# Optimization experiments

Measured on AMD Instinct MI355X. Metric: run time of the kernel, lower is better.

The kernel has to match this reference:

```python
import jax, jax.numpy as jnp
import numpy as np

N, E = 50000, 800000
IN_FEATS, EDGE_FEATS = 256, 64
H, F = 8, 32  # num_heads, out_feats
LRELU_SLOPE = 0.01  # nn.LeakyReLU() default (module ignores alpha arg)


def setup_inputs() -> dict:
    key = jax.random.key(0)
    ks = jax.random.split(key, 9)
    return {
        "h": jax.random.normal(ks[0], (N, IN_FEATS), jnp.float32),
        "edge_features": jax.random.normal(ks[1], (E, EDGE_FEATS), jnp.float32),
        "src": jax.random.randint(ks[2], (E,), 0, N, jnp.int32),
        "dst": jax.random.randint(ks[3], (E,), 0, N, jnp.int32),
        "W_w": jax.random.normal(ks[4], (IN_FEATS, H * F), jnp.float32) * 0.05,
        "We_w": jax.random.normal(ks[5], (EDGE_FEATS, H * F), jnp.float32) * 0.05,
        "a_src": jax.random.normal(ks[6], (H, F), jnp.float32) * 0.1,
        "a_dst": jax.random.normal(ks[7], (H, F), jnp.float32) * 0.1,
        "a_edge": jax.random.normal(ks[8], (H, F), jnp.float32) * 0.1,
    }


def reference(h, edge_features, src, dst, W_w, We_w, a_src, a_dst, a_edge):
    # Node / edge linear projections -> [N,H,F], [E,H,F]
    Wh = (h @ W_w).reshape(-1, H, F)
    We = (edge_features @ We_w).reshape(-1, H, F)

    # Per-edge attention logits [E,H]: score = src.a_src + dst.a_dst + e.a_edge
    s = (jnp.einsum('ehf,hf->eh', Wh[src], a_src)
         + jnp.einsum('ehf,hf->eh', Wh[dst], a_dst)
         + jnp.einsum('ehf,hf->eh', We, a_edge))
    s = jnp.where(s > 0, s, LRELU_SLOPE * s)

    # Segment softmax over incoming edges of each dst node
    m = jax.ops.segment_max(s, dst, num_segments=N)          # [N,H]
    ex = jnp.exp(s - m[dst])                                 # [E,H]
    den = jax.ops.segment_sum(ex, dst, num_segments=N)       # [N,H]
    a = ex / den[dst]                                        # [E,H]

    # Weighted scatter-sum aggregation (dropout is identity at p=0 / eval)
    msg = Wh[src] * a[:, :, None]                            # [E,H,F]
    h_new = jax.ops.segment_sum(msg, dst, num_segments=N)    # [N,H,F]

    # concat=True path: reshape + ELU
    h_new = h_new.reshape(-1, H * F)
    return jax.nn.elu(h_new)
```

## Files before the change

### kernel.cpp

```cpp
#include <hip/hip_runtime.h>
#include <hip/hip_fp16.h>

#define N_NODES 50000
#define N_EDGES 800000
#define HEADS 8
#define FOUT 32
#define HF 256
#define IN_F 256
#define EDGE_F 64
#define SCAN_BLOCKS 196
#define HIST_BLOCKS 3125
#define CVTW_BLOCKS 256

typedef __attribute__((ext_vector_type(8))) short bf16x8;
typedef __attribute__((ext_vector_type(4))) float f32x4;

__device__ inline ushort f2bf(float f) {
  unsigned u = __float_as_uint(f);
  unsigned r = 0x7FFFu + ((u >> 16) & 1u);
  return (ushort)((u + r) >> 16);
}

__global__ __launch_bounds__(256) void k_misc(
    const int* __restrict__ dst, int* __restrict__ deg,
    const float* __restrict__ W, ushort* __restrict__ Wt,
    const float* __restrict__ We_w, const float* __restrict__ a_edge,
    float* __restrict__ Bmat)
{
  int b = blockIdx.x;
  if (b < HIST_BLOCKS) {
    int e = b * 256 + threadIdx.x;
    atomicAdd(&deg[dst[e]], 1);
  } else if (b < HIST_BLOCKS + CVTW_BLOCKS) {
    int i = (b - HIST_BLOCKS) * 256 + threadIdx.x;
    int n = i >> 8, k = i & 255;
    Wt[i] = f2bf(W[k * HF + n]);
  } else {
    int i = (b - HIST_BLOCKS - CVTW_BLOCKS) * 256 + threadIdx.x;
    if (i < EDGE_F * HEADS) {
      int k = i >> 3, h = i & 7;
      float s = 0.f;
#pragma unroll
      for (int f = 0; f < FOUT; ++f)
        s += We_w[k * HF + h * FOUT + f] * a_edge[h * FOUT + f];
      Bmat[i] = s;
    }
  }
}

__global__ __launch_bounds__(256) void k_gemm_fused(
    const float* __restrict__ A,
    const ushort* __restrict__ Wt,
    const float* __restrict__ a_src, const float* __restrict__ a_dst,
    ushort* __restrict__ Whb,
    float* __restrict__ alpha_s, float* __restrict__ alpha_d, int M)
{
  __shared__ ushort As[64 * 40];
  __shared__ ushort Bs[256 * 40];
  const int tid = threadIdx.x;
  const int wave = tid >> 6, lane = tid & 63;
  const int m0 = blockIdx.x * 64;
  const int row16 = lane & 15;
  const int kg = lane >> 4;
  f32x4 acc[4][4] = {};

  const int a_r = tid >> 2;
  const int a_c = (tid & 3) * 8;
  const int a_row = m0 + a_r;

  for (int k0 = 0; k0 < IN_F; k0 += 32) {
    uint4 av = make_uint4(0, 0, 0, 0);
    if (a_row < M) {
      float4 f0 = *(const float4*)&A[(size_t)a_row * IN_F + k0 + a_c];
      float4 f1 = *(const float4*)&A[(size_t)a_row * IN_F + k0 + a_c + 4];
      av.x = (unsigned)f2bf(f0.x) | ((unsigned)f2bf(f0.y) << 16);
      av.y = (unsigned)f2bf(f0.z) | ((unsigned)f2bf(f0.w) << 16);
      av.z = (unsigned)f2bf(f1.x) | ((unsigned)f2bf(f1.y) << 16);
      av.w = (unsigned)f2bf(f1.z) | ((unsigned)f2bf(f1.w) << 16);
    }
    *(uint4*)&As[a_r * 40 + a_c] = av;
    const uint4* bp = (const uint4*)&Wt[(size_t)tid * IN_F + k0];
    uint4 b0 = bp[0], b1 = bp[1];
    *(uint4*)&Bs[tid * 40 + 0] = b0;
    *(uint4*)&Bs[tid * 40 + 8] = b1;
    uint4 b2 = bp[2], b3 = bp[3];
    *(uint4*)&Bs[tid * 40 + 16] = b2;
    *(uint4*)&Bs[tid * 40 + 24] = b3;
    __syncthreads();
    bf16x8 af[4], bfr[4];
#pragma unroll
    for (int mi = 0; mi < 4; ++mi)
      af[mi] = *(const bf16x8*)&As[(mi * 16 + row16) * 40 + kg * 8];
#pragma unroll
    for (int ni = 0; ni < 4; ++ni)
      bfr[ni] = *(const bf16x8*)&Bs[(wave * 64 + ni * 16 + row16) * 40 + kg * 8];
#pragma unroll
    for (int mi = 0; mi < 4; ++mi)
#pragma unroll
      for (int ni = 0; ni < 4; ++ni)
        acc[mi][ni] = __builtin_amdgcn_mfma_f32_16x16x32_bf16(af[mi], bfr[ni], acc[mi][ni], 0, 0, 0);
    __syncthreads();
  }

  float cs[4], cd[4];
#pragma unroll
  for (int ni = 0; ni < 4; ++ni) {
    int hh = 2 * wave + (ni >> 1);
    int ff = (ni & 1) * 16 + row16;
    cs[ni] = a_src[hh * FOUT + ff];
    cd[ni] = a_dst[hh * FOUT + ff];
  }
#pragma unroll
  for (int mi = 0; mi < 4; ++mi) {
#pragma unroll
    for (int r = 0; r < 4; ++r) {
      int row = m0 + mi * 16 + kg * 4 + r;
      float ps0 = acc[mi][0][r] * cs[0] + acc[mi][1][r] * cs[1];
      float ps1 = acc[mi][2][r] * cs[2] + acc[mi][3][r] * cs[3];
      float pd0 = acc[mi][0][r] * cd[0] + acc[mi][1][r] * cd[1];
      float pd1 = acc[mi][2][r] * cd[2] + acc[mi][3][r] * cd[3];
#pragma unroll
      for (int msk = 1; msk <= 8; msk <<= 1) {
        ps0 += __shfl_xor(ps0, msk, 64);
        ps1 += __shfl_xor(ps1, msk, 64);
        pd0 += __shfl_xor(pd0, msk, 64);
        pd1 += __shfl_xor(pd1, msk, 64);
      }
      if (row16 == 0 && row < M) {
        *(float2*)&alpha_s[row * 8 + 2 * wave] = make_float2(ps0, ps1);
        *(float2*)&alpha_d[row * 8 + 2 * wave] = make_float2(pd0, pd1);
      }
      if (row < M) {
#pragma unroll
        for (int ni = 0; ni < 4; ++ni)
          Whb[(size_t)row * HF + wave * 64 + ni * 16 + row16] = f2bf(acc[mi][ni][r]);
      }
    }
  }
}

__global__ __launch_bounds__(256) void k_scanA(const int* __restrict__ deg,
                                               int* __restrict__ blockSums)
{
  __shared__ int ws[4];
  int idx = blockIdx.x * 256 + threadIdx.x;
  int v = (idx < N_NODES) ? deg[idx] : 0;
  int s = v;
#pragma unroll
  for (int off = 32; off > 0; off >>= 1)
    s += __shfl_xor(s, off, 64);
  if ((threadIdx.x & 63) == 0) ws[threadIdx.x >> 6] = s;
  __syncthreads();
  if (threadIdx.x == 0)
    blockSums[blockIdx.x] = ws[0] + ws[1] + ws[2] + ws[3];
}

__global__ __launch_bounds__(256) void k_scanC(const int* __restrict__ deg,
                                               const int* __restrict__ blockSums,
                                               int* __restrict__ offsets,
                                               int* __restrict__ cursor)
{
  __shared__ int tmp[256];
  __shared__ int s_base;
  int t = threadIdx.x;
  int v = (t < SCAN_BLOCKS) ? blockSums[t] : 0;
  tmp[t] = v;
  __syncthreads();
  int x = v;
  for (int off = 1; off < 256; off <<= 1) {
    int y = (t >= off) ? tmp[t - off] : 0;
    __syncthreads();
    x += y;
    tmp[t] = x;
    __syncthreads();
  }
  if (t == (int)blockIdx.x) s_base = x - v;
  if (blockIdx.x == 0 && t == 255) offsets[N_NODES] = x;
  __syncthreads();
  int base = s_base;
  int idx = blockIdx.x * 256 + t;
  int d = (idx < N_NODES) ? deg[idx] : 0;
  tmp[t] = d;
  __syncthreads();
  int x2 = d;
  for (int off = 1; off < 256; off <<= 1) {
    int y = (t >= off) ? tmp[t - off] : 0;
    __syncthreads();
    x2 += y;
    tmp[t] = x2;
    __syncthreads();
  }
  if (idx < N_NODES) {
    int pre = base + x2 - d;
    offsets[idx] = pre;
    cursor[idx] = pre;
  }
}

__global__ __launch_bounds__(256) void k_sedge(
    const float* __restrict__ ef, const int* __restrict__ src,
    const int* __restrict__ dst, const float* __restrict__ alpha_s,
    const float* __restrict__ alpha_d, const float* __restrict__ Bmat,
    int* __restrict__ cursor, uint* __restrict__ s16u,
    int* __restrict__ srcN)
{
  __shared__ float Bs[EDGE_F * HEADS];
  for (int i = threadIdx.x; i < EDGE_F * HEADS; i += 256) Bs[i] = Bmat[i];
  __syncthreads();
  const int t = threadIdx.x;
  const int q = t & 3;
  const int e = blockIdx.x * 64 + (t >> 2);
  const int sn = src[e], dn = dst[e];

  float sc[8] = {};
  const float4* efr = (const float4*)&ef[(size_t)e * EDGE_F + q * 16];
#pragma unroll
  for (int g = 0; g < 4; ++g) {
    float4 v = efr[g];
    const float* b0 = &Bs[(q * 16 + g * 4) * 8];
#pragma unroll
    for (int hh = 0; hh < 8; ++hh)
      sc[hh] += v.x * b0[hh] + v.y * b0[8 + hh] + v.z * b0[16 + hh] + v.w * b0[24 + hh];
  }
#pragma unroll
  for (int hh = 0; hh < 8; ++hh) {
    sc[hh] += __shfl_xor(sc[hh], 1, 64);
    sc[hh] += __shfl_xor(sc[hh], 2, 64);
  }
  float2 as = *(const float2*)&alpha_s[sn * 8 + 2 * q];
  float2 ad = *(const float2*)&alpha_d[dn * 8 + 2 * q];
  float a0 = sc[2 * q] + as.x + ad.x;
  float a1 = sc[2 * q + 1] + as.y + ad.y;
  a0 = a0 > 0.f ? a0 : 0.01f * a0;
  a1 = a1 > 0.f ? a1 : 0.01f * a1;
  uint hv = (uint)__half_as_ushort(__float2half_rn(a0)) |
            ((uint)__half_as_ushort(__float2half_rn(a1)) << 16);
  int p = 0;
  if (q == 0) p = atomicAdd(&cursor[dn], 1);
  p = __shfl(p, t & 60, 64);
  s16u[(size_t)p * 4 + q] = hv;
  if (q == 0) srcN[p] = sn;
}

__global__ __launch_bounds__(256) void k_agg(
    const ushort* __restrict__ s16, const int* __restrict__ srcN,
    const int* __restrict__ offsets, const uint* __restrict__ Whb_u,
    float* __restrict__ out)
{
  const int n = blockIdx.x * 4 + (threadIdx.x >> 6);
  const int l = threadIdx.x & 63;
  const int beg = offsets[n], end = offsets[n + 1];
  const int es = l >> 3;
  const int h0 = l >> 4;
  const int h1 = 4 + h0;

  float m_run = -3.0e38f, l_run = 0.f;
  float acc00 = 0.f, acc01 = 0.f, acc10 = 0.f, acc11 = 0.f;

  int rx = 0;
  float s_cur = -3.0e38f;
  if (beg + es < end) {
    rx = srcN[beg + es];
    s_cur = __half2float(((const __half*)s16)[(size_t)beg * 8 + l]);
  }

  for (int c0 = beg; c0 < end; c0 += 8) {
    const int cnt = min(8, end - c0);
    int rx_n = 0;
    float s_n = -3.0e38f;
    if (c0 + 8 + es < end) {
      rx_n = srcN[c0 + 8 + es];
      s_n = __half2float(((const __half*)s16)[(size_t)(c0 + 8) * 8 + l]);
    }
    float s = s_cur;
    float mc = s;
    mc = fmaxf(mc, __shfl_xor(mc, 8, 64));
    mc = fmaxf(mc, __shfl_xor(mc, 16, 64));
    mc = fmaxf(mc, __shfl_xor(mc, 32, 64));
    float m_new = fmaxf(m_run, mc);
    float f = __expf(m_run - m_new);
    float w = __expf(s - m_new);
    float ws = w;
    ws += __shfl_xor(ws, 8, 64);
    ws += __shfl_xor(ws, 16, 64);
    ws += __shfl_xor(ws, 32, 64);
    l_run = l_run * f + ws;
    m_run = m_new;
    float f0 = __shfl(f, h0, 64);
    float f1 = __shfl(f, h1, 64);
    acc00 *= f0; acc01 *= f0; acc10 *= f1; acc11 *= f1;
    if (cnt == 8) {
#pragma unroll
      for (int k = 0; k < 8; ++k) {
        int idx = __shfl(rx, k << 3, 64);
        float w0 = __shfl(w, (k << 3) | h0, 64);
        float w1 = __shfl(w, (k << 3) | h1, 64);
        const uint* rowp = Whb_u + ((size_t)idx << 7);
        uint v0 = rowp[l];
        uint v1 = rowp[l + 64];
        acc00 = fmaf(w0, __uint_as_float(v0 << 16), acc00);
        acc01 = fmaf(w0, __uint_as_float(v0 & 0xFFFF0000u), acc01);
        acc10 = fmaf(w1, __uint_as_float(v1 << 16), acc10);
        acc11 = fmaf(w1, __uint_as_float(v1 & 0xFFFF0000u), acc11);
      }
    } else {
      for (int k = 0; k < cnt; ++k) {
        int idx = __shfl(rx, k << 3, 64);
        float w0 = __shfl(w, (k << 3) | h0, 64);
        float w1 = __shfl(w, (k << 3) | h1, 64);
        const uint* rowp = Whb_u + ((size_t)idx << 7);
        uint v0 = rowp[l];
        uint v1 = rowp[l + 64];
        acc00 = fmaf(w0, __uint_as_float(v0 << 16), acc00);
        acc01 = fmaf(w0, __uint_as_float(v0 & 0xFFFF0000u), acc01);
        acc10 = fmaf(w1, __uint_as_float(v1 << 16), acc10);
        acc11 = fmaf(w1, __uint_as_float(v1 & 0xFFFF0000u), acc11);
      }
    }
    rx = rx_n;
    s_cur = s_n;
  }

  float l0 = __shfl(l_run, h0, 64);
  float l1 = __shfl(l_run, h1, 64);
  float inv0 = (l0 > 0.f) ? 1.f / l0 : 0.f;
  float inv1 = (l1 > 0.f) ? 1.f / l1 : 0.f;
  acc00 *= inv0; acc01 *= inv0; acc10 *= inv1; acc11 *= inv1;

  float2 oA, oB;
  oA.x = acc00 > 0.f ? acc00 : expm1f(acc00);
  oA.y = acc01 > 0.f ? acc01 : expm1f(acc01);
  oB.x = acc10 > 0.f ? acc10 : expm1f(acc10);
  oB.y = acc11 > 0.f ? acc11 : expm1f(acc11);
  *(float2*)&out[(size_t)n * HF + 2 * l] = oA;
  *(float2*)&out[(size_t)n * HF + 128 + 2 * l] = oB;
}

extern "C" void kernel_launch(void* const* d_in, const int* in_sizes, int n_in,
                              void* d_out, int out_size, void* d_ws, size_t ws_size,
                              hipStream_t stream)
{
  const float* h    = (const float*)d_in[0];
  const float* ef   = (const float*)d_in[1];
  const int*   src  = (const int*)d_in[2];
  const int*   dst  = (const int*)d_in[3];
  const float* W_w  = (const float*)d_in[4];
  const float* We_w = (const float*)d_in[5];
  const float* a_s  = (const float*)d_in[6];
  const float* a_d  = (const float*)d_in[7];
  const float* a_e  = (const float*)d_in[8];
  float* out = (float*)d_out;

  char* ws = (char*)d_ws;
  size_t off = 0;
  auto take = [&](size_t bytes) {
    char* p = ws + off;
    off += (bytes + 255) & ~(size_t)255;
    return p;
  };
  ushort* Whb     = (ushort*)take((size_t)N_NODES * HF * 2);
  uint*   s16u    = (uint*)take((size_t)N_EDGES * 8 * 2);
  float* alpha_s  = (float*)take((size_t)N_NODES * HEADS * 4);
  float* alpha_d  = (float*)take((size_t)N_NODES * HEADS * 4);
  int*   srcN     = (int*)take((size_t)N_EDGES * 4);
  int*   deg      = (int*)take((size_t)N_NODES * 4);
  int*   offs     = (int*)take((size_t)(N_NODES + 1) * 4);
  int*   cursor   = (int*)take((size_t)N_NODES * 4);
  float* Bmat     = (float*)take((size_t)EDGE_F * HEADS * 4);
  ushort* Wt      = (ushort*)take((size_t)HF * IN_F * 2);
  int*   blockSums= (int*)take((size_t)SCAN_BLOCKS * 4);

  (void)hipMemsetAsync(deg, 0, N_NODES * sizeof(int), stream);
  k_misc<<<HIST_BLOCKS + CVTW_BLOCKS + 2, 256, 0, stream>>>(dst, deg, W_w, Wt,
                                                            We_w, a_e, Bmat);
  k_scanA<<<SCAN_BLOCKS, 256, 0, stream>>>(deg, blockSums);
  k_scanC<<<SCAN_BLOCKS, 256, 0, stream>>>(deg, blockSums, offs, cursor);
  k_gemm_fused<<<(N_NODES + 63) / 64, 256, 0, stream>>>(h, Wt, a_s, a_d, Whb,
                                                        alpha_s, alpha_d, N_NODES);
  k_sedge<<<N_EDGES / 64, 256, 0, stream>>>(ef, src, dst, alpha_s, alpha_d,
                                            Bmat, cursor, s16u, srcN);
  k_agg<<<N_NODES / 4, 256, 0, stream>>>((const ushort*)s16u, srcN, offs,
                                         (const uint*)Whb, out);
}
```

Measured before the change: 242.8 us.

## Fuse scan-A into GEMM launch, process two edges per thread, widen agg loads

The block-sum scan kernel is folded into the GEMM launch as extra blocks, which removes one kernel launch and lets the scan overlap with GEMM work. The edge-score kernel now handles two edges per thread group, halving its grid and adding memory-level parallelism at the cost of more registers. The aggregation kernel maps each lane to four contiguous features of one head and uses 8-byte loads with one float4 store, replacing two strided 4-byte loads and two float2 stores. This cuts shuffle and instruction count per edge.

```diff
diff --git a/kernel.cpp b/kernel.cpp
--- a/kernel.cpp
+++ b/kernel.cpp
@@ -11,6 +11,7 @@
 #define SCAN_BLOCKS 196
 #define HIST_BLOCKS 3125
 #define CVTW_BLOCKS 256
+#define GEMM_BLOCKS 782
 
 typedef __attribute__((ext_vector_type(8))) short bf16x8;
 typedef __attribute__((ext_vector_type(4))) float f32x4;
@@ -53,8 +54,25 @@
     const ushort* __restrict__ Wt,
     const float* __restrict__ a_src, const float* __restrict__ a_dst,
     ushort* __restrict__ Whb,
-    float* __restrict__ alpha_s, float* __restrict__ alpha_d, int M)
-{
+    float* __restrict__ alpha_s, float* __restrict__ alpha_d,
+    const int* __restrict__ deg, int* __restrict__ blockSums, int M)
+{
+  if (blockIdx.x >= GEMM_BLOCKS) {
+    __shared__ int ws4[4];
+    int b2 = blockIdx.x - GEMM_BLOCKS;
+    int idx = b2 * 256 + threadIdx.x;
+    int v = (idx < N_NODES) ? deg[idx] : 0;
+    int s = v;
+#pragma unroll
+    for (int off = 32; off > 0; off >>= 1)
+      s += __shfl_xor(s, off, 64);
+    if ((threadIdx.x & 63) == 0) ws4[threadIdx.x >> 6] = s;
+    __syncthreads();
+    if (threadIdx.x == 0)
+      blockSums[b2] = ws4[0] + ws4[1] + ws4[2] + ws4[3];
+    return;
+  }
+
   __shared__ ushort As[64 * 40];
   __shared__ ushort Bs[256 * 40];
   const int tid = threadIdx.x;
@@ -139,22 +157,6 @@
   }
 }
 
-__global__ __launch_bounds__(256) void k_scanA(const int* __restrict__ deg,
-                                               int* __restrict__ blockSums)
-{
-  __shared__ int ws[4];
-  int idx = blockIdx.x * 256 + threadIdx.x;
-  int v = (idx < N_NODES) ? deg[idx] : 0;
-  int s = v;
-#pragma unroll
-  for (int off = 32; off > 0; off >>= 1)
-    s += __shfl_xor(s, off, 64);
-  if ((threadIdx.x & 63) == 0) ws[threadIdx.x >> 6] = s;
-  __syncthreads();
-  if (threadIdx.x == 0)
-    blockSums[blockIdx.x] = ws[0] + ws[1] + ws[2] + ws[3];
-}
-
 __global__ __launch_bounds__(256) void k_scanC(const int* __restrict__ deg,
                                                const int* __restrict__ blockSums,
                                                int* __restrict__ offsets,
@@ -209,53 +211,77 @@
   __syncthreads();
   const int t = threadIdx.x;
   const int q = t & 3;
-  const int e = blockIdx.x * 64 + (t >> 2);
-  const int sn = src[e], dn = dst[e];
-
-  float sc[8] = {};
-  const float4* efr = (const float4*)&ef[(size_t)e * EDGE_F + q * 16];
-#pragma unroll
-  for (int g = 0; g < 4; ++g) {
-    float4 v = efr[g];
-    const float* b0 = &Bs[(q * 16 + g * 4) * 8];
-#pragma unroll
-    for (int hh = 0; hh < 8; ++hh)
-      sc[hh] += v.x * b0[hh] + v.y * b0[8 + hh] + v.z * b0[16 + hh] + v.w * b0[24 + hh];
-  }
+  const int e0 = blockIdx.x * 128 + (t >> 2);
+  const int e1 = e0 + 64;
+  const int sn0 = src[e0], dn0 = dst[e0];
+  const int sn1 = src[e1], dn1 = dst[e1];
+
+  const float4* ep0 = (const float4*)&ef[(size_t)e0 * EDGE_F + q * 16];
+  const float4* ep1 = (const float4*)&ef[(size_t)e1 * EDGE_F + q * 16];
+  float4 v0a = ep0[0], v0b = ep0[1], v0c = ep0[2], v0d = ep0[3];
+  float4 v1a = ep1[0], v1b = ep1[1], v1c = ep1[2], v1d = ep1[3];
+
+  float sc0[8] = {}, sc1[8] = {};
+  const float* bb = &Bs[q * 16 * 8];
 #pragma unroll
   for (int hh = 0; hh < 8; ++hh) {
-    sc[hh] += __shfl_xor(sc[hh], 1, 64);
-    sc[hh] += __shfl_xor(sc[hh], 2, 64);
-  }
-  float2 as = *(const float2*)&alpha_s[sn * 8 + 2 * q];
-  float2 ad = *(const float2*)&alpha_d[dn * 8 + 2 * q];
-  float a0 = sc[2 * q] + as.x + ad.x;
-  float a1 = sc[2 * q + 1] + as.y + ad.y;
-  a0 = a0 > 0.f ? a0 : 0.01f * a0;
-  a1 = a1 > 0.f ? a1 : 0.01f * a1;
-  uint hv = (uint)__half_as_ushort(__float2half_rn(a0)) |
-            ((uint)__half_as_ushort(__float2half_rn(a1)) << 16);
-  int p = 0;
-  if (q == 0) p = atomicAdd(&cursor[dn], 1);
-  p = __shfl(p, t & 60, 64);
-  s16u[(size_t)p * 4 + q] = hv;
-  if (q == 0) srcN[p] = sn;
+    sc0[hh] += v0a.x * bb[hh]      + v0a.y * bb[8 + hh]  + v0a.z * bb[16 + hh] + v0a.w * bb[24 + hh];
+    sc1[hh] += v1a.x * bb[hh]      + v1a.y * bb[8 + hh]  + v1a.z * bb[16 + hh] + v1a.w * bb[24 + hh];
+    sc0[hh] += v0b.x * bb[32 + hh] + v0b.y * bb[40 + hh] + v0b.z * bb[48 + hh] + v0b.w * bb[56 + hh];
+    sc1[hh] += v1b.x * bb[32 + hh] + v1b.y * bb[40 + hh] + v1b.z * bb[48 + hh] + v1b.w * bb[56 + hh];
+    sc0[hh] += v0c.x * bb[64 + hh] + v0c.y * bb[72 + hh] + v0c.z * bb[80 + hh] + v0c.w * bb[88 + hh];
+    sc1[hh] += v1c.x * bb[64 + hh] + v1c.y * bb[72 + hh] + v1c.z * bb[80 + hh] + v1c.w * bb[88 + hh];
+    sc0[hh] += v0d.x * bb[96 + hh] + v0d.y * bb[104 + hh]+ v0d.z * bb[112 + hh]+ v0d.w * bb[120 + hh];
+    sc1[hh] += v1d.x * bb[96 + hh] + v1d.y * bb[104 + hh]+ v1d.z * bb[112 + hh]+ v1d.w * bb[120 + hh];
+  }
+#pragma unroll
+  for (int hh = 0; hh < 8; ++hh) {
+    sc0[hh] += __shfl_xor(sc0[hh], 1, 64);
+    sc0[hh] += __shfl_xor(sc0[hh], 2, 64);
+    sc1[hh] += __shfl_xor(sc1[hh], 1, 64);
+    sc1[hh] += __shfl_xor(sc1[hh], 2, 64);
+  }
+  float2 as0 = *(const float2*)&alpha_s[sn0 * 8 + 2 * q];
+  float2 ad0 = *(const float2*)&alpha_d[dn0 * 8 + 2 * q];
+  float2 as1 = *(const float2*)&alpha_s[sn1 * 8 + 2 * q];
+  float2 ad1 = *(const float2*)&alpha_d[dn1 * 8 + 2 * q];
+  float a00 = sc0[2 * q] + as0.x + ad0.x;
+  float a01 = sc0[2 * q + 1] + as0.y + ad0.y;
+  float a10 = sc1[2 * q] + as1.x + ad1.x;
+  float a11 = sc1[2 * q + 1] + as1.y + ad1.y;
+  a00 = a00 > 0.f ? a00 : 0.01f * a00;
+  a01 = a01 > 0.f ? a01 : 0.01f * a01;
+  a10 = a10 > 0.f ? a10 : 0.01f * a10;
+  a11 = a11 > 0.f ? a11 : 0.01f * a11;
+  uint hv0 = (uint)__half_as_ushort(__float2half_rn(a00)) |
+             ((uint)__half_as_ushort(__float2half_rn(a01)) << 16);
+  uint hv1 = (uint)__half_as_ushort(__float2half_rn(a10)) |
+             ((uint)__half_as_ushort(__float2half_rn(a11)) << 16);
+  int p0 = 0, p1 = 0;
+  if (q == 0) {
+    p0 = atomicAdd(&cursor[dn0], 1);
+    p1 = atomicAdd(&cursor[dn1], 1);
+  }
+  p0 = __shfl(p0, t & 60, 64);
+  p1 = __shfl(p1, t & 60, 64);
+  s16u[(size_t)p0 * 4 + q] = hv0;
+  s16u[(size_t)p1 * 4 + q] = hv1;
+  if (q == 0) { srcN[p0] = sn0; srcN[p1] = sn1; }
 }
 
 __global__ __launch_bounds__(256) void k_agg(
     const ushort* __restrict__ s16, const int* __restrict__ srcN,
-    const int* __restrict__ offsets, const uint* __restrict__ Whb_u,
+    const int* __restrict__ offsets, const uint2* __restrict__ Whb_u2,
     float* __restrict__ out)
 {
   const int n = blockIdx.x * 4 + (threadIdx.x >> 6);
   const int l = threadIdx.x & 63;
   const int beg = offsets[n], end = offsets[n + 1];
   const int es = l >> 3;
-  const int h0 = l >> 4;
-  const int h1 = 4 + h0;
+  const int h = l >> 3;
 
   float m_run = -3.0e38f, l_run = 0.f;
-  float acc00 = 0.f, acc01 = 0.f, acc10 = 0.f, acc11 = 0.f;
+  float a0 = 0.f, a1 = 0.f, a2 = 0.f, a3 = 0.f;
 
   int rx = 0;
   float s_cur = -3.0e38f;
@@ -286,54 +312,44 @@
     ws += __shfl_xor(ws, 32, 64);
     l_run = l_run * f + ws;
     m_run = m_new;
-    float f0 = __shfl(f, h0, 64);
-    float f1 = __shfl(f, h1, 64);
-    acc00 *= f0; acc01 *= f0; acc10 *= f1; acc11 *= f1;
+    float fh = __shfl(f, h, 64);
+    a0 *= fh; a1 *= fh; a2 *= fh; a3 *= fh;
     if (cnt == 8) {
 #pragma unroll
       for (int k = 0; k < 8; ++k) {
         int idx = __shfl(rx, k << 3, 64);
-        float w0 = __shfl(w, (k << 3) | h0, 64);
-        float w1 = __shfl(w, (k << 3) | h1, 64);
-        const uint* rowp = Whb_u + ((size_t)idx << 7);
-        uint v0 = rowp[l];
-        uint v1 = rowp[l + 64];
-        acc00 = fmaf(w0, __uint_as_float(v0 << 16), acc00);
-        acc01 = fmaf(w0, __uint_as_float(v0 & 0xFFFF0000u), acc01);
-        acc10 = fmaf(w1, __uint_as_float(v1 << 16), acc10);
-        acc11 = fmaf(w1, __uint_as_float(v1 & 0xFFFF0000u), acc11);
+        float wk = __shfl(w, (k << 3) | h, 64);
+        uint2 v = Whb_u2[((size_t)idx << 6) + l];
+        a0 = fmaf(wk, __uint_as_float(v.x << 16), a0);
+        a1 = fmaf(wk, __uint_as_float(v.x & 0xFFFF0000u), a1);
+        a2 = fmaf(wk, __uint_as_float(v.y << 16), a2);
+        a3 = fmaf(wk, __uint_as_float(v.y & 0xFFFF0000u), a3);
       }
     } else {
       for (int k = 0; k < cnt; ++k) {
         int idx = __shfl(rx, k << 3, 64);
-        float w0 = __shfl(w, (k << 3) | h0, 64);
-        float w1 = __shfl(w, (k << 3) | h1, 64);
-        const uint* rowp = Whb_u + ((size_t)idx << 7);
-        uint v0 = rowp[l];
-        uint v1 = rowp[l + 64];
-        acc00 = fmaf(w0, __uint_as_float(v0 << 16), acc00);
-        acc01 = fmaf(w0, __uint_as_float(v0 & 0xFFFF0000u), acc01);
-        acc10 = fmaf(w1, __uint_as_float(v1 << 16), acc10);
-        acc11 = fmaf(w1, __uint_as_float(v1 & 0xFFFF0000u), acc11);
+        float wk = __shfl(w, (k << 3) | h, 64);
+        uint2 v = Whb_u2[((size_t)idx << 6) + l];
+        a0 = fmaf(wk, __uint_as_float(v.x << 16), a0);
+        a1 = fmaf(wk, __uint_as_float(v.x & 0xFFFF0000u), a1);
+        a2 = fmaf(wk, __uint_as_float(v.y << 16), a2);
+        a3 = fmaf(wk, __uint_as_float(v.y & 0xFFFF0000u), a3);
       }
     }
     rx = rx_n;
     s_cur = s_n;
   }
 
-  float l0 = __shfl(l_run, h0, 64);
-  float l1 = __shfl(l_run, h1, 64);
-  float inv0 = (l0 > 0.f) ? 1.f / l0 : 0.f;
-  float inv1 = (l1 > 0.f) ? 1.f / l1 : 0.f;
-  acc00 *= inv0; acc01 *= inv0; acc10 *= inv1; acc11 *= inv1;
-
-  float2 oA, oB;
-  oA.x = acc00 > 0.f ? acc00 : expm1f(acc00);
-  oA.y = acc01 > 0.f ? acc01 : expm1f(acc01);
-  oB.x = acc10 > 0.f ? acc10 : expm1f(acc10);
-  oB.y = acc11 > 0.f ? acc11 : expm1f(acc11);
-  *(float2*)&out[(size_t)n * HF + 2 * l] = oA;
-  *(float2*)&out[(size_t)n * HF + 128 + 2 * l] = oB;
+  float lh = __shfl(l_run, h, 64);
+  float inv = (lh > 0.f) ? 1.f / lh : 0.f;
+  a0 *= inv; a1 *= inv; a2 *= inv; a3 *= inv;
+
+  float4 o;
+  o.x = a0 > 0.f ? a0 : expm1f(a0);
+  o.y = a1 > 0.f ? a1 : expm1f(a1);
+  o.z = a2 > 0.f ? a2 : expm1f(a2);
+  o.w = a3 > 0.f ? a3 : expm1f(a3);
+  *(float4*)&out[(size_t)n * HF + 4 * l] = o;
 }
 
 extern "C" void kernel_launch(void* const* d_in, const int* in_sizes, int n_in,
@@ -373,12 +389,12 @@
   (void)hipMemsetAsync(deg, 0, N_NODES * sizeof(int), stream);
   k_misc<<<HIST_BLOCKS + CVTW_BLOCKS + 2, 256, 0, stream>>>(dst, deg, W_w, Wt,
                                                             We_w, a_e, Bmat);
-  k_scanA<<<SCAN_BLOCKS, 256, 0, stream>>>(deg, blockSums);
+  k_gemm_fused<<<GEMM_BLOCKS + SCAN_BLOCKS, 256, 0, stream>>>(h, Wt, a_s, a_d, Whb,
+                                                              alpha_s, alpha_d,
+                                                              deg, blockSums, N_NODES);
   k_scanC<<<SCAN_BLOCKS, 256, 0, stream>>>(deg, blockSums, offs, cursor);
-  k_gemm_fused<<<(N_NODES + 63) / 64, 256, 0, stream>>>(h, Wt, a_s, a_d, Whb,
-                                                        alpha_s, alpha_d, N_NODES);
-  k_sedge<<<N_EDGES / 64, 256, 0, stream>>>(ef, src, dst, alpha_s, alpha_d,
-                                            Bmat, cursor, s16u, srcN);
+  k_sedge<<<N_EDGES / 128, 256, 0, stream>>>(ef, src, dst, alpha_s, alpha_d,
+                                             Bmat, cursor, s16u, srcN);
   k_agg<<<N_NODES / 4, 256, 0, stream>>>((const ushort*)s16u, srcN, offs,
-                                         (const uint*)Whb, out);
-}
+                                         (const uint2*)Whb, out);
+}
```

Measured after the change: 249.9 us. 1.03x slower.
